# Kernel tuning notes

Measured on AMD Instinct MI355X. Metric: run time of the kernel, lower is better.

## Reference

```python
import jax, jax.numpy as jnp
import numpy as np

B, S, D = 2, 2048, 1024   # batch, seq, token_dim
H, E = 16, 64             # heads, embedding_size per head


def setup_inputs() -> dict:
    key = jax.random.key(0)
    ks = jax.random.split(key, 5)
    x = jax.random.normal(ks[0], (B, S, D), dtype=jnp.float32)
    attention_mask = jnp.ones((B, S), dtype=jnp.int32)  # accepted but unused, as in source
    # torch.rand -> uniform [0,1)
    w_queries = jax.random.uniform(ks[1], (H, D, E), dtype=jnp.float32)
    w_keys = jax.random.uniform(ks[2], (H, D, E), dtype=jnp.float32)
    w_values = jax.random.uniform(ks[3], (H, D, E), dtype=jnp.float32)
    w_agg = jax.random.uniform(ks[4], (H * E, D), dtype=jnp.float32)
    return {"x": x, "attention_mask": attention_mask, "w_queries": w_queries,
            "w_keys": w_keys, "w_values": w_values, "w_agg": w_agg}


def reference(x, attention_mask, w_queries, w_keys, w_values, w_agg):
    # Batched over all heads at once (original loops in Python per head).
    q = jnp.einsum('bsd,hde->bhse', x, w_queries)  # [B,H,S,E]
    k = jnp.einsum('bsd,hde->bhse', x, w_keys)
    v = jnp.einsum('bsd,hde->bhse', x, w_values)
    scores = jnp.einsum('bhse,bhte->bhst', q, k) / jnp.sqrt(jnp.float32(E))  # [B,H,S,S]
    # NOTE: source applies softmax over dim=1 of the per-head [B,S,S] scores,
    # i.e. over the QUERY axis (axis=2 here), not the usual key axis.
    attn = jax.nn.softmax(scores, axis=2)
    heads = jnp.einsum('bhst,bhte->bhse', attn, v)  # [B,H,S,E]
    # concat along last dim in head order -> [B,S,H*E]
    multi = jnp.transpose(heads, (0, 2, 1, 3)).reshape(B, S, H * E)
    return multi @ w_agg  # [B,S,D]
```

## Files before the change

kernel.cpp:

```cpp
#include <hip/hip_runtime.h>
#include <hip/hip_bf16.h>


typedef __attribute__((ext_vector_type(8))) short bf16x8;
typedef __attribute__((ext_vector_type(4))) float f32x4;

#define C1 0.18033688011112042f

__device__ __forceinline__ unsigned short f2bf(float f){
  union { __hip_bfloat16 h; unsigned short u; } cv;
  cv.h = __float2bfloat16(f);
  return cv.u;
}
__device__ __forceinline__ unsigned int pk2(float a, float b){
  union { __hip_bfloat162 h; unsigned int u; } cv;
  cv.h = __float22bfloat162_rn(make_float2(a, b));
  return cv.u;
}
__device__ __forceinline__ unsigned long long pack4(float a, float b, float c, float d){
  return (unsigned long long)pk2(a, b) | ((unsigned long long)pk2(c, d) << 32);
}
__device__ __forceinline__ float bf2f(unsigned short u){
  unsigned int x = ((unsigned int)u) << 16;
  return __builtin_bit_cast(float, x);
}

#define GLOAD16(SRC, DST)                                                        \
  __builtin_amdgcn_global_load_lds(                                              \
      (const __attribute__((address_space(1))) void*)(SRC),                      \
      (__attribute__((address_space(3))) void*)(DST), 16, 0, 0)

__global__ void k_cvt_x(const float* __restrict__ in, unsigned short* __restrict__ out){
  int i = (blockIdx.x * 256 + threadIdx.x) * 4;
  float4 v = *reinterpret_cast<const float4*>(in + i);
  *reinterpret_cast<unsigned long long*>(out + i) = pack4(v.x, v.y, v.z, v.w);
}

__global__ void k_cvt_w3(const float* __restrict__ wq, const float* __restrict__ wk,
                         const float* __restrict__ wv, unsigned short* __restrict__ out){
  int z = blockIdx.y;
  const float* w = (z == 0) ? wq : ((z == 1) ? wk : wv);
  int o = blockIdx.x * 256 + threadIdx.x;
  int he = o >> 10, d = o & 1023;
  int h = he >> 6, e = he & 63;
  out[((size_t)z << 20) + o] = f2bf(w[(h << 16) + (d << 6) + e]);
}

__global__ void k_cvt_wagg(const float* __restrict__ w, unsigned short* __restrict__ out){
  int o = blockIdx.x * 256 + threadIdx.x;
  int d = o >> 11, c = o & 2047, he = c & 1023;
  out[o] = f2bf(w[(he << 10) + d]);
}

__global__ __launch_bounds__(256) void k_proj(const unsigned short* __restrict__ Wall,
                                              const unsigned short* __restrict__ Xb,
                                              unsigned short* __restrict__ Qb,
                                              unsigned short* __restrict__ Kb,
                                              unsigned short* __restrict__ Vt){
  __shared__ __align__(16) unsigned short lds[2][2][4096];
  const int z = blockIdx.z;
  const unsigned short* Wt = Wall + ((size_t)z << 20);
  const int t = threadIdx.x;
  const int w = t >> 6, lane = t & 63, g = lane >> 4, cl = lane & 15;
  const int wn = w >> 1, wm = w & 1;
  const int n0 = blockIdx.x * 128, m0 = blockIdx.y * 128;

  const int rowS = t & 127;
  const unsigned short* sA = Wt + (size_t)(n0 + rowS) * 1024 + (t >> 7) * 8;
  const unsigned short* sB = Xb + (size_t)(m0 + rowS) * 1024 + (t >> 7) * 8;

  f32x4 acc[4][4];
#pragma unroll
  for (int i = 0; i < 4; ++i)
#pragma unroll
    for (int j = 0; j < 4; ++j) acc[i][j] = f32x4{0.f, 0.f, 0.f, 0.f};

  GLOAD16(sA,      &lds[0][0][t * 8]);
  GLOAD16(sA + 16, &lds[0][0][t * 8 + 2048]);
  GLOAD16(sB,      &lds[0][1][t * 8]);
  GLOAD16(sB + 16, &lds[0][1][t * 8 + 2048]);
  __syncthreads();

#pragma unroll 2
  for (int kt = 0; kt < 32; ++kt){
    const int cur = kt & 1;
    if (kt < 31){
      const unsigned short* nA = sA + (kt + 1) * 32;
      const unsigned short* nB = sB + (kt + 1) * 32;
      GLOAD16(nA,      &lds[cur ^ 1][0][t * 8]);
      GLOAD16(nA + 16, &lds[cur ^ 1][0][t * 8 + 2048]);
      GLOAD16(nB,      &lds[cur ^ 1][1][t * 8]);
      GLOAD16(nB + 16, &lds[cur ^ 1][1][t * 8 + 2048]);
    }
    const unsigned short* la = &lds[cur][0][g * 1024];
    const unsigned short* lb = &lds[cur][1][g * 1024];
    bf16x8 af[4], bq[4];
#pragma unroll
    for (int i = 0; i < 4; ++i) af[i] = *(const bf16x8*)(la + (wn * 64 + i * 16 + cl) * 8);
#pragma unroll
    for (int j = 0; j < 4; ++j) bq[j] = *(const bf16x8*)(lb + (wm * 64 + j * 16 + cl) * 8);
#pragma unroll
    for (int i = 0; i < 4; ++i)
#pragma unroll
      for (int j = 0; j < 4; ++j)
        acc[i][j] = __builtin_amdgcn_mfma_f32_16x16x32_bf16(af[i], bq[j], acc[i][j], 0, 0, 0);
    __syncthreads();
  }

  const float scale = (z == 0) ? C1 : 1.f;
#pragma unroll
  for (int i = 0; i < 4; ++i)
#pragma unroll
    for (int j = 0; j < 4; ++j)
#pragma unroll
      for (int jj = 0; jj < 4; ++jj) acc[i][j][jj] *= scale;

  if (z < 2){
    unsigned short* outp = (z == 0) ? Qb : Kb;
#pragma unroll
    for (int i = 0; i < 4; ++i)
#pragma unroll
      for (int j = 0; j < 4; ++j){
        int m = m0 + wm * 64 + 16 * j + cl;
        int n = n0 + wn * 64 + 16 * i + 4 * g;
        *reinterpret_cast<unsigned long long*>(outp + (size_t)m * 1024 + n) =
            pack4(acc[i][j][0], acc[i][j][1], acc[i][j][2], acc[i][j][3]);
      }
  } else {
    int b = m0 >> 11;
#pragma unroll
    for (int i = 0; i < 4; ++i)
#pragma unroll
      for (int j = 0; j < 4; ++j){
        int c2 = (m0 & 2047) + wm * 64 + 16 * j + cl;
        int nb = b * 1024 + n0 + wn * 64 + 16 * i + 4 * g;
#pragma unroll
        for (int jj = 0; jj < 4; ++jj)
          Vt[(size_t)(nb + jj) * 2048 + c2] = f2bf(acc[i][j][jj]);
      }
  }
}

__global__ __launch_bounds__(256) void k_agg(const unsigned short* __restrict__ Wa,
                                             const unsigned short* __restrict__ Hd,
                                             float* __restrict__ outp){
  __shared__ __align__(16) unsigned short lds[2][2][4096];
  const int t = threadIdx.x;
  const int w = t >> 6, lane = t & 63, g = lane >> 4, cl = lane & 15;
  const int wn = w >> 1, wm = w & 1;
  const int n0 = blockIdx.x * 128, m0 = blockIdx.y * 128;

  const int rowS = t & 127;
  const unsigned short* sA = Wa + (size_t)(n0 + rowS) * 2048 + (t >> 7) * 8;
  const unsigned short* sB = Hd + (size_t)(m0 + rowS) * 2048 + (t >> 7) * 8;

  f32x4 acc[4][4];
#pragma unroll
  for (int i = 0; i < 4; ++i)
#pragma unroll
    for (int j = 0; j < 4; ++j) acc[i][j] = f32x4{0.f, 0.f, 0.f, 0.f};

  GLOAD16(sA,      &lds[0][0][t * 8]);
  GLOAD16(sA + 16, &lds[0][0][t * 8 + 2048]);
  GLOAD16(sB,      &lds[0][1][t * 8]);
  GLOAD16(sB + 16, &lds[0][1][t * 8 + 2048]);
  __syncthreads();

#pragma unroll 2
  for (int kt = 0; kt < 64; ++kt){
    const int cur = kt & 1;
    if (kt < 63){
      const unsigned short* nA = sA + (kt + 1) * 32;
      const unsigned short* nB = sB + (kt + 1) * 32;
      GLOAD16(nA,      &lds[cur ^ 1][0][t * 8]);
      GLOAD16(nA + 16, &lds[cur ^ 1][0][t * 8 + 2048]);
      GLOAD16(nB,      &lds[cur ^ 1][1][t * 8]);
      GLOAD16(nB + 16, &lds[cur ^ 1][1][t * 8 + 2048]);
    }
    const unsigned short* la = &lds[cur][0][g * 1024];
    const unsigned short* lb = &lds[cur][1][g * 1024];
    bf16x8 af[4], bq[4];
#pragma unroll
    for (int i = 0; i < 4; ++i) af[i] = *(const bf16x8*)(la + (wn * 64 + i * 16 + cl) * 8);
#pragma unroll
    for (int j = 0; j < 4; ++j) bq[j] = *(const bf16x8*)(lb + (wm * 64 + j * 16 + cl) * 8);
#pragma unroll
    for (int i = 0; i < 4; ++i)
#pragma unroll
      for (int j = 0; j < 4; ++j)
        acc[i][j] = __builtin_amdgcn_mfma_f32_16x16x32_bf16(af[i], bq[j], acc[i][j], 0, 0, 0);
    __syncthreads();
  }
#pragma unroll
  for (int i = 0; i < 4; ++i)
#pragma unroll
    for (int j = 0; j < 4; ++j){
      int m = m0 + wm * 64 + 16 * j + cl;
      int n = n0 + wn * 64 + 16 * i + 4 * g;
      *reinterpret_cast<f32x4*>(outp + (size_t)m * 1024 + n) = acc[i][j];
    }
}

__global__ __launch_bounds__(256, 4) void k_stats(const unsigned short* __restrict__ Qb,
                                                  const unsigned short* __restrict__ Kb,
                                                  float* __restrict__ mp,
                                                  float* __restrict__ lp){
  __shared__ __align__(16) unsigned short Qs[2][64][64];
  const int B = blockIdx.x;
  const int xcd = B & 7, rest = B >> 3;
  const int tx = rest & 7, gi = rest >> 3;
  const int grp = xcd + 8 * gi;
  const int bh = grp & 31, z = grp >> 5;
  const int b = bh >> 4, h = bh & 15;
  const int w = threadIdx.x >> 6, lane = threadIdx.x & 63;
  const int g = lane >> 4, cl = lane & 15;
  const int t0 = tx * 256 + w * 64;

  const unsigned short* kp = Kb + (size_t)(b * 2048 + t0 + cl) * 1024 + h * 64 + g * 8;
  bf16x8 a[4][2];
#pragma unroll
  for (int ti = 0; ti < 4; ++ti){
    a[ti][0] = *(const bf16x8*)(kp + (size_t)ti * 16 * 1024);
    a[ti][1] = *(const bf16x8*)(kp + (size_t)ti * 16 * 1024 + 32);
  }

  const int r0 = threadIdx.x >> 3, sl = threadIdx.x & 7;
  const unsigned short* qsrc = Qb + (size_t)(b * 2048 + z * 512 + r0) * 1024 + h * 64
                               + ((sl ^ (r0 & 7)) * 8);
  unsigned short* qdst0 = &Qs[0][0][0] + threadIdx.x * 8;

  const int e0 = (g ^ (cl & 7)) * 8;
  const int e1 = ((g + 4) ^ (cl & 7)) * 8;

  float m[16], l[16];
#pragma unroll
  for (int i = 0; i < 16; ++i){ m[i] = -3.0e38f; l[i] = 0.f; }

  GLOAD16(qsrc,               qdst0);
  GLOAD16(qsrc + 32 * 1024,   qdst0 + 2048);
  __syncthreads();
  for (int c = 0; c < 8; ++c){
    const int buf = c & 1;
    if (c < 7){
      const unsigned short* s2 = qsrc + (size_t)(c + 1) * 64 * 1024;
      unsigned short* d2 = qdst0 + (buf ^ 1) * 4096;
      GLOAD16(s2,             d2);
      GLOAD16(s2 + 32 * 1024, d2 + 2048);
    }
#pragma unroll
    for (int st = 0; st < 4; ++st){
      const unsigned short* qrow = &Qs[buf][st * 16 + cl][0];
      bf16x8 b0 = *(const bf16x8*)(qrow + e0);
      bf16x8 b1 = *(const bf16x8*)(qrow + e1);
#pragma unroll
      for (int ti = 0; ti < 4; ++ti){
        f32x4 zz = {0.f, 0.f, 0.f, 0.f};
        f32x4 d = __builtin_amdgcn_mfma_f32_16x16x32_bf16(a[ti][0], b0, zz, 0, 0, 0);
        d = __builtin_amdgcn_mfma_f32_16x16x32_bf16(a[ti][1], b1, d, 0, 0, 0);
#pragma unroll
        for (int j = 0; j < 4; ++j) m[ti * 4 + j] = fmaxf(m[ti * 4 + j], d[j]);
      }
    }
    __syncthreads();
  }
#pragma unroll
  for (int off = 1; off < 16; off <<= 1)
#pragma unroll
    for (int i = 0; i < 16; ++i) m[i] = fmaxf(m[i], __shfl_xor(m[i], off));

  GLOAD16(qsrc,               qdst0);
  GLOAD16(qsrc + 32 * 1024,   qdst0 + 2048);
  __syncthreads();
  for (int c = 0; c < 8; ++c){
    const int buf = c & 1;
    if (c < 7){
      const unsigned short* s2 = qsrc + (size_t)(c + 1) * 64 * 1024;
      unsigned short* d2 = qdst0 + (buf ^ 1) * 4096;
      GLOAD16(s2,             d2);
      GLOAD16(s2 + 32 * 1024, d2 + 2048);
    }
#pragma unroll
    for (int st = 0; st < 4; ++st){
      const unsigned short* qrow = &Qs[buf][st * 16 + cl][0];
      bf16x8 b0 = *(const bf16x8*)(qrow + e0);
      bf16x8 b1 = *(const bf16x8*)(qrow + e1);
#pragma unroll
      for (int ti = 0; ti < 4; ++ti){
        f32x4 zz = {0.f, 0.f, 0.f, 0.f};
        f32x4 d = __builtin_amdgcn_mfma_f32_16x16x32_bf16(a[ti][0], b0, zz, 0, 0, 0);
        d = __builtin_amdgcn_mfma_f32_16x16x32_bf16(a[ti][1], b1, d, 0, 0, 0);
#pragma unroll
        for (int j = 0; j < 4; ++j) l[ti * 4 + j] += exp2f(d[j] - m[ti * 4 + j]);
      }
    }
    __syncthreads();
  }
#pragma unroll
  for (int off = 1; off < 16; off <<= 1)
#pragma unroll
    for (int i = 0; i < 16; ++i) l[i] += __shfl_xor(l[i], off);

  if (cl == 0){
    size_t base = ((size_t)z * 32 + bh) * 2048 + t0;
#pragma unroll
    for (int ti = 0; ti < 4; ++ti){
      f32x4 mv = {m[ti * 4 + 0], m[ti * 4 + 1], m[ti * 4 + 2], m[ti * 4 + 3]};
      f32x4 lv = {l[ti * 4 + 0], l[ti * 4 + 1], l[ti * 4 + 2], l[ti * 4 + 3]};
      *(f32x4*)(mp + base + ti * 16 + 4 * g) = mv;
      *(f32x4*)(lp + base + ti * 16 + 4 * g) = lv;
    }
  }
}

__global__ void k_mcomb(const float* __restrict__ mp, const float* __restrict__ lp,
                        float* __restrict__ m2, float* __restrict__ rl){
  int i = blockIdx.x * 256 + threadIdx.x;
  float m0 = mp[i], m1 = mp[65536 + i], m2v = mp[131072 + i], m3 = mp[196608 + i];
  float l0 = lp[i], l1 = lp[65536 + i], l2 = lp[131072 + i], l3 = lp[196608 + i];
  float m = fmaxf(fmaxf(m0, m1), fmaxf(m2v, m3));
  float l = l0 * exp2f(m0 - m) + l1 * exp2f(m1 - m)
          + l2 * exp2f(m2v - m) + l3 * exp2f(m3 - m);
  m2[i] = m;
  rl[i] = 1.f / l;
}

__global__ void k_scale_v(unsigned short* __restrict__ Vt, const float* __restrict__ rl){
  int row = blockIdx.x;
  int b = row >> 10, h = (row >> 6) & 15;
  int t = threadIdx.x * 8;
  const float* r = rl + (size_t)(b * 16 + h) * 2048 + t;
  unsigned short* p = Vt + (size_t)row * 2048 + t;
  bf16x8 v = *(const bf16x8*)p;
  f32x4 r0 = *(const f32x4*)r;
  f32x4 r1 = *(const f32x4*)(r + 4);
  float f[8];
#pragma unroll
  for (int j = 0; j < 8; ++j) f[j] = bf2f((unsigned short)v[j]);
#pragma unroll
  for (int j = 0; j < 4; ++j){ f[j] *= r0[j]; f[4 + j] *= r1[j]; }
  unsigned long long* q = (unsigned long long*)p;
  q[0] = pack4(f[0], f[1], f[2], f[3]);
  q[1] = pack4(f[4], f[5], f[6], f[7]);
}

__global__ __launch_bounds__(256, 4) void k_attn(const unsigned short* __restrict__ Qb,
                                                 const unsigned short* __restrict__ Kb,
                                                 const unsigned short* __restrict__ Vt,
                                                 const float* __restrict__ m2,
                                                 unsigned short* __restrict__ Hd){
  __shared__ __align__(16) unsigned short Ks[2][32][64];
  __shared__ __align__(16) unsigned short Vs2[2][64][32];
  __shared__ unsigned short Pl[4][32][40];
  const int B = blockIdx.x;
  const int xcd = B & 7, rest = B >> 3;
  const int sx = rest & 15, gi = rest >> 4;
  const int grp = xcd + 8 * gi;
  const int bh = grp & 31, z = grp >> 5;
  const int b = bh >> 4, h = bh & 15;
  const int w = threadIdx.x >> 6, lane = threadIdx.x & 63;
  const int g = lane >> 4, cl = lane & 15;
  const int s0w = sx * 128 + w * 32;
  const int tbase = z * 1024;

  bf16x8 q[2][2];
#pragma unroll
  for (int ss = 0; ss < 2; ++ss){
    const unsigned short* qp = Qb + (size_t)(b * 2048 + s0w + ss * 16 + cl) * 1024 + h * 64 + g * 8;
    q[ss][0] = *(const bf16x8*)(qp);
    q[ss][1] = *(const bf16x8*)(qp + 32);
  }
  f32x4 acc[4][2];
#pragma unroll
  for (int i = 0; i < 4; ++i)
#pragma unroll
    for (int ss = 0; ss < 2; ++ss) acc[i][ss] = f32x4{0.f, 0.f, 0.f, 0.f};

  const int kr = threadIdx.x >> 3, ksl = threadIdx.x & 7;
  const unsigned short* kStage = Kb + (size_t)(b * 2048 + tbase + kr) * 1024 + h * 64
                                 + ((ksl ^ (kr & 7)) * 8);
  const int vr = threadIdx.x >> 2, vsl = threadIdx.x & 3;
  const unsigned short* vStage = Vt + (size_t)(b * 1024 + h * 64 + vr) * 2048 + tbase
                                 + ((vsl ^ (vr & 3)) * 8);
  unsigned short* kDst = &Ks[0][0][0] + threadIdx.x * 8;
  unsigned short* vDst = &Vs2[0][0][0] + threadIdx.x * 8;

  const float* mb = m2 + (size_t)bh * 2048 + tbase + 4 * g;
  const int eK = (g ^ (cl & 7)) * 8;
  const int eK2 = ((g + 4) ^ (cl & 7)) * 8;
  const int eV = (g ^ (cl & 3)) * 8;

  GLOAD16(kStage, kDst);
  GLOAD16(vStage, vDst);
  __syncthreads();

  for (int c = 0; c < 32; ++c){
    const int buf = c & 1;
    if (c < 31){
      GLOAD16(kStage + (size_t)(c + 1) * 32 * 1024, kDst + (buf ^ 1) * 2048);
      GLOAD16(vStage + (c + 1) * 32,                vDst + (buf ^ 1) * 2048);
    }
#pragma unroll
    for (int tile = 0; tile < 2; ++tile){
      const unsigned short* krow = &Ks[buf][tile * 16 + cl][0];
      bf16x8 a0 = *(const bf16x8*)(krow + eK);
      bf16x8 a1 = *(const bf16x8*)(krow + eK2);
      f32x4 mv = *(const f32x4*)(mb + c * 32 + tile * 16);
#pragma unroll
      for (int ss = 0; ss < 2; ++ss){
        f32x4 zz = {0.f, 0.f, 0.f, 0.f};
        f32x4 d = __builtin_amdgcn_mfma_f32_16x16x32_bf16(a0, q[ss][0], zz, 0, 0, 0);
        d = __builtin_amdgcn_mfma_f32_16x16x32_bf16(a1, q[ss][1], d, 0, 0, 0);
        float p0 = exp2f(d[0] - mv[0]);
        float p1 = exp2f(d[1] - mv[1]);
        float p2 = exp2f(d[2] - mv[2]);
        float p3 = exp2f(d[3] - mv[3]);
        *reinterpret_cast<unsigned long long*>(&Pl[w][ss * 16 + cl][tile * 16 + 4 * g]) =
            pack4(p0, p1, p2, p3);
      }
    }
    bf16x8 bp0 = *(const bf16x8*)(&Pl[w][cl][g * 8]);
    bf16x8 bp1 = *(const bf16x8*)(&Pl[w][16 + cl][g * 8]);
#pragma unroll
    for (int i = 0; i < 4; ++i){
      bf16x8 av = *(const bf16x8*)(&Vs2[buf][16 * i + cl][0] + eV);
      acc[i][0] = __builtin_amdgcn_mfma_f32_16x16x32_bf16(av, bp0, acc[i][0], 0, 0, 0);
      acc[i][1] = __builtin_amdgcn_mfma_f32_16x16x32_bf16(av, bp1, acc[i][1], 0, 0, 0);
    }
    __syncthreads();
  }
#pragma unroll
  for (int i = 0; i < 4; ++i)
#pragma unroll
    for (int ss = 0; ss < 2; ++ss){
      *reinterpret_cast<unsigned long long*>(
          Hd + (size_t)(b * 2048 + s0w + ss * 16 + cl) * 2048 + z * 1024 + h * 64 + 16 * i + 4 * g) =
          pack4(acc[i][ss][0], acc[i][ss][1], acc[i][ss][2], acc[i][ss][3]);
    }
}

extern "C" void kernel_launch(void* const* d_in, const int* in_sizes, int n_in,
                              void* d_out, int out_size, void* d_ws, size_t ws_size,
                              hipStream_t stream) {
  const float* x    = (const float*)d_in[0];
  const float* wq   = (const float*)d_in[2];
  const float* wk   = (const float*)d_in[3];
  const float* wv   = (const float*)d_in[4];
  const float* wagg = (const float*)d_in[5];
  float* outp = (float*)d_out;

  char* ws = (char*)d_ws;
  unsigned short* Xb  = (unsigned short*)(ws);
  unsigned short* Hd  = (unsigned short*)(ws);
  unsigned short* Wall= (unsigned short*)(ws + 16777216);
  float* mp = (float*)(ws + 16777216);
  float* lp = (float*)(ws + 17825792);
  float* m2 = (float*)(ws + 18874368);
  float* rl = (float*)(ws + 19136512);
  unsigned short* Wat = (unsigned short*)(ws + 23068672);
  unsigned short* Qb  = (unsigned short*)(ws + 27262976);
  unsigned short* Kb  = (unsigned short*)(ws + 35651584);
  unsigned short* Vt  = (unsigned short*)(ws + 44040192);

  k_cvt_x   <<<dim3(4096),    dim3(256), 0, stream>>>(x, Xb);
  k_cvt_w3  <<<dim3(4096, 3), dim3(256), 0, stream>>>(wq, wk, wv, Wall);
  k_cvt_wagg<<<dim3(8192),    dim3(256), 0, stream>>>(wagg, Wat);

  k_proj<<<dim3(8, 32, 3), dim3(256), 0, stream>>>(Wall, Xb, Qb, Kb, Vt);

  k_stats  <<<dim3(1024), dim3(256), 0, stream>>>(Qb, Kb, mp, lp);
  k_mcomb  <<<dim3(256),  dim3(256), 0, stream>>>(mp, lp, m2, rl);
  k_scale_v<<<dim3(2048), dim3(256), 0, stream>>>(Vt, rl);

  k_attn<<<dim3(1024), dim3(256), 0, stream>>>(Qb, Kb, Vt, m2, Hd);
  k_agg <<<dim3(8, 32), dim3(256), 0, stream>>>(Wat, Hd, outp);
}
```

Measured before the change: 267.0 us.

## Tile weight transposes through LDS, fold max into MFMA init, permlane P repack

The weight conversion kernels now transpose through an LDS tile, so global reads are coalesced float4 loads and writes are vectorized 16-byte bf16 stores, replacing strided scalar accesses. In the stats and attention kernels, the subtraction of the row max is folded into the MFMA accumulator init, which removes a per-element subtract before exp2. In the attention kernel, the LDS round trip that rearranged the P tile into B-operand layout is replaced by in-register permlane32/permlane16 swaps, and the Pl shared buffer is removed. The swaps fall back to shuffles when the builtins are missing, and the new lane mapping must exactly match the MFMA operand layout to stay correct.

```diff
diff --git a/kernel.cpp b/kernel.cpp
--- a/kernel.cpp
+++ b/kernel.cpp
@@ -25,6 +25,29 @@
   return __builtin_bit_cast(float, x);
 }
 
+__device__ __forceinline__ void swap32(unsigned a, unsigned b, unsigned &x, unsigned &y){
+#if __has_builtin(__builtin_amdgcn_permlane32_swap)
+  auto r = __builtin_amdgcn_permlane32_swap(a, b, false, false);
+  x = r[0]; y = r[1];
+#else
+  int lane = threadIdx.x & 63;
+  unsigned as = __shfl_xor((int)a, 32), bs = __shfl_xor((int)b, 32);
+  x = (lane & 32) ? bs : a;
+  y = (lane & 32) ? b : as;
+#endif
+}
+__device__ __forceinline__ void swap16(unsigned a, unsigned b, unsigned &x, unsigned &y){
+#if __has_builtin(__builtin_amdgcn_permlane16_swap)
+  auto r = __builtin_amdgcn_permlane16_swap(a, b, false, false);
+  x = r[0]; y = r[1];
+#else
+  int lane = threadIdx.x & 63;
+  unsigned as = __shfl_xor((int)a, 16), bs = __shfl_xor((int)b, 16);
+  x = (lane & 16) ? bs : a;
+  y = (lane & 16) ? b : as;
+#endif
+}
+
 #define GLOAD16(SRC, DST)                                                        \
   __builtin_amdgcn_global_load_lds(                                              \
       (const __attribute__((address_space(1))) void*)(SRC),                      \
@@ -36,20 +59,58 @@
   *reinterpret_cast<unsigned long long*>(out + i) = pack4(v.x, v.y, v.z, v.w);
 }
 
-__global__ void k_cvt_w3(const float* __restrict__ wq, const float* __restrict__ wk,
-                         const float* __restrict__ wv, unsigned short* __restrict__ out){
-  int z = blockIdx.y;
-  const float* w = (z == 0) ? wq : ((z == 1) ? wk : wv);
-  int o = blockIdx.x * 256 + threadIdx.x;
-  int he = o >> 10, d = o & 1023;
-  int h = he >> 6, e = he & 63;
-  out[((size_t)z << 20) + o] = f2bf(w[(h << 16) + (d << 6) + e]);
-}
-
-__global__ void k_cvt_wagg(const float* __restrict__ w, unsigned short* __restrict__ out){
-  int o = blockIdx.x * 256 + threadIdx.x;
-  int d = o >> 11, c = o & 2047, he = c & 1023;
-  out[o] = f2bf(w[(he << 10) + d]);
+__global__ __launch_bounds__(256) void k_cvt_w3t(const float* __restrict__ wq,
+                                                 const float* __restrict__ wk,
+                                                 const float* __restrict__ wv,
+                                                 unsigned short* __restrict__ out){
+  __shared__ unsigned short T[64][72];
+  const int z = blockIdx.z;
+  const float* w = ((z == 0) ? wq : ((z == 1) ? wk : wv)) + ((size_t)blockIdx.y << 16);
+  const int d0 = blockIdx.x * 64;
+  const int r = threadIdx.x >> 2, c0 = (threadIdx.x & 3) << 4;
+  const float* src = w + ((size_t)(d0 + r) << 6) + c0;
+#pragma unroll
+  for (int i = 0; i < 4; ++i){
+    float4 v = *(const float4*)(src + 4 * i);
+    T[r][c0 + 4 * i + 0] = f2bf(v.x);
+    T[r][c0 + 4 * i + 1] = f2bf(v.y);
+    T[r][c0 + 4 * i + 2] = f2bf(v.z);
+    T[r][c0 + 4 * i + 3] = f2bf(v.w);
+  }
+  __syncthreads();
+  const int e = threadIdx.x >> 2, k0 = (threadIdx.x & 3) << 4;
+  union { unsigned short s[8]; bf16x8 v; } u0, u1;
+#pragma unroll
+  for (int k = 0; k < 8; ++k){ u0.s[k] = T[k0 + k][e]; u1.s[k] = T[k0 + 8 + k][e]; }
+  unsigned short* dst = out + ((size_t)z << 20) + (((size_t)blockIdx.y * 64 + e) << 10) + d0 + k0;
+  *(bf16x8*)dst = u0.v;
+  *(bf16x8*)(dst + 8) = u1.v;
+}
+
+__global__ __launch_bounds__(256) void k_cvt_waggt(const float* __restrict__ w,
+                                                   unsigned short* __restrict__ out){
+  __shared__ unsigned short T[64][72];
+  const int d0 = blockIdx.x * 64, he0 = blockIdx.y * 64;
+  const int r = threadIdx.x >> 2, c0 = (threadIdx.x & 3) << 4;
+  const float* src = w + ((size_t)(he0 + r) << 10) + d0 + c0;
+#pragma unroll
+  for (int i = 0; i < 4; ++i){
+    float4 v = *(const float4*)(src + 4 * i);
+    T[r][c0 + 4 * i + 0] = f2bf(v.x);
+    T[r][c0 + 4 * i + 1] = f2bf(v.y);
+    T[r][c0 + 4 * i + 2] = f2bf(v.z);
+    T[r][c0 + 4 * i + 3] = f2bf(v.w);
+  }
+  __syncthreads();
+  const int d = threadIdx.x >> 2, k0 = (threadIdx.x & 3) << 4;
+  union { unsigned short s[8]; bf16x8 v; } u0, u1;
+#pragma unroll
+  for (int k = 0; k < 8; ++k){ u0.s[k] = T[k0 + k][d]; u1.s[k] = T[k0 + 8 + k][d]; }
+  unsigned short* dst = out + ((size_t)(d0 + d) << 11) + he0 + k0;
+  *(bf16x8*)dst = u0.v;
+  *(bf16x8*)(dst + 8) = u1.v;
+  *(bf16x8*)(dst + 1024) = u0.v;
+  *(bf16x8*)(dst + 1032) = u1.v;
 }
 
 __global__ __launch_bounds__(256) void k_proj(const unsigned short* __restrict__ Wall,
@@ -236,8 +297,8 @@
 #pragma unroll
   for (int i = 0; i < 16; ++i){ m[i] = -3.0e38f; l[i] = 0.f; }
 
-  GLOAD16(qsrc,               qdst0);
-  GLOAD16(qsrc + 32 * 1024,   qdst0 + 2048);
+  GLOAD16(qsrc,             qdst0);
+  GLOAD16(qsrc + 32 * 1024, qdst0 + 2048);
   __syncthreads();
   for (int c = 0; c < 8; ++c){
     const int buf = c & 1;
@@ -268,8 +329,14 @@
 #pragma unroll
     for (int i = 0; i < 16; ++i) m[i] = fmaxf(m[i], __shfl_xor(m[i], off));
 
-  GLOAD16(qsrc,               qdst0);
-  GLOAD16(qsrc + 32 * 1024,   qdst0 + 2048);
+  f32x4 ci[4];
+#pragma unroll
+  for (int ti = 0; ti < 4; ++ti)
+#pragma unroll
+    for (int j = 0; j < 4; ++j) ci[ti][j] = -m[ti * 4 + j];
+
+  GLOAD16(qsrc,             qdst0);
+  GLOAD16(qsrc + 32 * 1024, qdst0 + 2048);
   __syncthreads();
   for (int c = 0; c < 8; ++c){
     const int buf = c & 1;
@@ -286,11 +353,10 @@
       bf16x8 b1 = *(const bf16x8*)(qrow + e1);
 #pragma unroll
       for (int ti = 0; ti < 4; ++ti){
-        f32x4 zz = {0.f, 0.f, 0.f, 0.f};
-        f32x4 d = __builtin_amdgcn_mfma_f32_16x16x32_bf16(a[ti][0], b0, zz, 0, 0, 0);
+        f32x4 d = __builtin_amdgcn_mfma_f32_16x16x32_bf16(a[ti][0], b0, ci[ti], 0, 0, 0);
         d = __builtin_amdgcn_mfma_f32_16x16x32_bf16(a[ti][1], b1, d, 0, 0, 0);
 #pragma unroll
-        for (int j = 0; j < 4; ++j) l[ti * 4 + j] += exp2f(d[j] - m[ti * 4 + j]);
+        for (int j = 0; j < 4; ++j) l[ti * 4 + j] += exp2f(d[j]);
       }
     }
     __syncthreads();
@@ -350,16 +416,15 @@
                                                  unsigned short* __restrict__ Hd){
   __shared__ __align__(16) unsigned short Ks[2][32][64];
   __shared__ __align__(16) unsigned short Vs2[2][64][32];
-  __shared__ unsigned short Pl[4][32][40];
   const int B = blockIdx.x;
   const int xcd = B & 7, rest = B >> 3;
   const int sx = rest & 15, gi = rest >> 4;
   const int grp = xcd + 8 * gi;
   const int bh = grp & 31, z = grp >> 5;
   const int b = bh >> 4, h = bh & 15;
-  const int w = threadIdx.x >> 6, lane = threadIdx.x & 63;
+  const int lane = threadIdx.x & 63;
   const int g = lane >> 4, cl = lane & 15;
-  const int s0w = sx * 128 + w * 32;
+  const int s0w = sx * 128 + (threadIdx.x >> 6) * 32;
   const int tbase = z * 1024;
 
   bf16x8 q[2][2];
@@ -399,32 +464,42 @@
       GLOAD16(kStage + (size_t)(c + 1) * 32 * 1024, kDst + (buf ^ 1) * 2048);
       GLOAD16(vStage + (c + 1) * 32,                vDst + (buf ^ 1) * 2048);
     }
-#pragma unroll
-    for (int tile = 0; tile < 2; ++tile){
-      const unsigned short* krow = &Ks[buf][tile * 16 + cl][0];
-      bf16x8 a0 = *(const bf16x8*)(krow + eK);
-      bf16x8 a1 = *(const bf16x8*)(krow + eK2);
-      f32x4 mv = *(const f32x4*)(mb + c * 32 + tile * 16);
-#pragma unroll
-      for (int ss = 0; ss < 2; ++ss){
-        f32x4 zz = {0.f, 0.f, 0.f, 0.f};
-        f32x4 d = __builtin_amdgcn_mfma_f32_16x16x32_bf16(a0, q[ss][0], zz, 0, 0, 0);
-        d = __builtin_amdgcn_mfma_f32_16x16x32_bf16(a1, q[ss][1], d, 0, 0, 0);
-        float p0 = exp2f(d[0] - mv[0]);
-        float p1 = exp2f(d[1] - mv[1]);
-        float p2 = exp2f(d[2] - mv[2]);
-        float p3 = exp2f(d[3] - mv[3]);
-        *reinterpret_cast<unsigned long long*>(&Pl[w][ss * 16 + cl][tile * 16 + 4 * g]) =
-            pack4(p0, p1, p2, p3);
-      }
-    }
-    bf16x8 bp0 = *(const bf16x8*)(&Pl[w][cl][g * 8]);
-    bf16x8 bp1 = *(const bf16x8*)(&Pl[w][16 + cl][g * 8]);
+    const unsigned short* kr0 = &Ks[buf][cl][0];
+    const unsigned short* kr1 = &Ks[buf][16 + cl][0];
+    bf16x8 a00 = *(const bf16x8*)(kr0 + eK);
+    bf16x8 a01 = *(const bf16x8*)(kr0 + eK2);
+    bf16x8 a10 = *(const bf16x8*)(kr1 + eK);
+    bf16x8 a11 = *(const bf16x8*)(kr1 + eK2);
+    f32x4 mv0 = *(const f32x4*)(mb + c * 32);
+    f32x4 mv1 = *(const f32x4*)(mb + c * 32 + 16);
+    f32x4 ci0 = {-mv0[0], -mv0[1], -mv0[2], -mv0[3]};
+    f32x4 ci1 = {-mv1[0], -mv1[1], -mv1[2], -mv1[3]};
+
+    bf16x8 pb[2];
+#pragma unroll
+    for (int ss = 0; ss < 2; ++ss){
+      f32x4 d0 = __builtin_amdgcn_mfma_f32_16x16x32_bf16(a00, q[ss][0], ci0, 0, 0, 0);
+      d0 = __builtin_amdgcn_mfma_f32_16x16x32_bf16(a01, q[ss][1], d0, 0, 0, 0);
+      f32x4 d1 = __builtin_amdgcn_mfma_f32_16x16x32_bf16(a10, q[ss][0], ci1, 0, 0, 0);
+      d1 = __builtin_amdgcn_mfma_f32_16x16x32_bf16(a11, q[ss][1], d1, 0, 0, 0);
+      unsigned w00 = pk2(exp2f(d0[0]), exp2f(d0[1]));
+      unsigned w01 = pk2(exp2f(d0[2]), exp2f(d0[3]));
+      unsigned w10 = pk2(exp2f(d1[0]), exp2f(d1[1]));
+      unsigned w11 = pk2(exp2f(d1[2]), exp2f(d1[3]));
+      unsigned sa0, sb0, sa1, sb1, W0, W1, W2, W3;
+      swap32(w00, w10, sa0, sb0);
+      swap32(w01, w11, sa1, sb1);
+      swap16(sa0, sb0, W0, W2);
+      swap16(sa1, sb1, W1, W3);
+      union { unsigned u[4]; bf16x8 v; } fr;
+      fr.u[0] = W0; fr.u[1] = W1; fr.u[2] = W2; fr.u[3] = W3;
+      pb[ss] = fr.v;
+    }
 #pragma unroll
     for (int i = 0; i < 4; ++i){
       bf16x8 av = *(const bf16x8*)(&Vs2[buf][16 * i + cl][0] + eV);
-      acc[i][0] = __builtin_amdgcn_mfma_f32_16x16x32_bf16(av, bp0, acc[i][0], 0, 0, 0);
-      acc[i][1] = __builtin_amdgcn_mfma_f32_16x16x32_bf16(av, bp1, acc[i][1], 0, 0, 0);
+      acc[i][0] = __builtin_amdgcn_mfma_f32_16x16x32_bf16(av, pb[0], acc[i][0], 0, 0, 0);
+      acc[i][1] = __builtin_amdgcn_mfma_f32_16x16x32_bf16(av, pb[1], acc[i][1], 0, 0, 0);
     }
     __syncthreads();
   }
@@ -461,9 +536,9 @@
   unsigned short* Kb  = (unsigned short*)(ws + 35651584);
   unsigned short* Vt  = (unsigned short*)(ws + 44040192);
 
-  k_cvt_x   <<<dim3(4096),    dim3(256), 0, stream>>>(x, Xb);
-  k_cvt_w3  <<<dim3(4096, 3), dim3(256), 0, stream>>>(wq, wk, wv, Wall);
-  k_cvt_wagg<<<dim3(8192),    dim3(256), 0, stream>>>(wagg, Wat);
+  k_cvt_x    <<<dim3(4096),       dim3(256), 0, stream>>>(x, Xb);
+  k_cvt_w3t  <<<dim3(16, 16, 3),  dim3(256), 0, stream>>>(wq, wk, wv, Wall);
+  k_cvt_waggt<<<dim3(16, 16),     dim3(256), 0, stream>>>(wagg, Wat);
 
   k_proj<<<dim3(8, 32, 3), dim3(256), 0, stream>>>(Wall, Xb, Qb, Kb, Vt);
 
```

Measured after the change: 352.0 us. 1.32x slower.
